# Kernel optimization log

Hardware: AMD Instinct MI355X
Metric: run time of the kernel (lower is better)

## Reference

```python
import jax, jax.numpy as jnp
import numpy as np

NUM_HEADS = 8
NEG_SLOPE = 0.2
MASK_VAL = -10000000000.0


def setup_inputs() -> dict:
    key = jax.random.key(0)
    k1, k2, k3, k4 = jax.random.split(key, 4)
    B, N, H, d, T = 16, 256, NUM_HEADS, 64, 5
    src = jax.random.normal(k1, (B, N, H * d), dtype=jnp.float32)
    dst = jax.random.normal(k2, (B, N, H * d), dtype=jnp.float32)
    # parameter a: (atom_d*H, atom_d, T); xavier-ish scale
    a = jax.random.normal(k3, (H * d, d, T), dtype=jnp.float32) * 0.08
    # bond-type indices in [-1, T); -1 = no edge (masked)
    edges = jax.random.randint(k4, (B, N, N), -1, T, dtype=jnp.int64)
    return {"src_embeddings": src, "dst_embeddings": dst, "a": a, "edges": edges}


def reference(src_embeddings, dst_embeddings, a, edges):
    B, N, d_ = src_embeddings.shape
    H = NUM_HEADS
    d = d_ // H
    T = a.shape[-1]
    # (B, H, N, d)
    s = src_embeddings.reshape(B, N, H, d).transpose(0, 2, 1, 3)
    t = dst_embeddings.reshape(B, N, H, d).transpose(0, 2, 1, 3)
    # a.view(H, d, d*T) in torch == reshape(H, d, d, T) with (e, t) flattened
    A = a.reshape(H, d, d, T)
    # transformed_src[b,h,i,e,t] = sum_d s[b,h,i,d] * A[h,d,e,t]
    transformed = jnp.einsum('bhid,hdet->bhiet', s, A)
    # scores[b,h,i,j,t] = sum_e transformed[b,h,i,e,t] * t[b,h,j,e]  -> (B,H,N,N,T)
    scores = jnp.einsum('bhiet,bhje->bhijt', transformed, t)
    # gather the per-edge bond-type slice
    idx = jnp.broadcast_to(jnp.clip(edges, 0)[:, None, :, :, None], (B, H, N, N, 1))
    sel = jnp.take_along_axis(scores, idx, axis=-1)[..., 0]  # (B,H,N,N)
    mask = (edges == -1)[:, None, :, :]
    sel = jnp.where(mask, jnp.asarray(MASK_VAL, sel.dtype), sel)
    return jax.nn.leaky_relu(sel, negative_slope=NEG_SLOPE)
```

## Files before the change

### kernel.cpp

```cpp
#include <hip/hip_runtime.h>
#include <hip/hip_bf16.h>

#define NB 16
#define NN 256
#define NH 8
#define ND 64
#define NT 5
#define HD 512

typedef __bf16 bf16x8 __attribute__((ext_vector_type(8)));
typedef __bf16 bf16x4 __attribute__((ext_vector_type(4)));
typedef float  f32x4  __attribute__((ext_vector_type(4)));
typedef int    i32x4  __attribute__((ext_vector_type(4)));

__device__ __forceinline__ bf16x8 cvt8(f32x4 a, f32x4 b) {
    bf16x8 r;
    r[0] = (__bf16)a[0]; r[1] = (__bf16)a[1]; r[2] = (__bf16)a[2]; r[3] = (__bf16)a[3];
    r[4] = (__bf16)b[0]; r[5] = (__bf16)b[1]; r[6] = (__bf16)b[2]; r[7] = (__bf16)b[3];
    return r;
}

__device__ __forceinline__ void stage16(const void* g, void* l) {
    __builtin_amdgcn_global_load_lds(
        (const __attribute__((address_space(1))) void*)g,
        (__attribute__((address_space(3))) void*)l,
        16, 0, 0);
}

__global__ void prep_w_kernel(const float* __restrict__ a, __bf16* __restrict__ wt) {
    const int o8 = (blockIdx.x * 256 + threadIdx.x) * 8;
    if (o8 >= NH * ND * ND * NT) return;
    const int dd0 = o8 & 63;
    const int e   = (o8 >> 6) & 63;
    const int ht  = o8 >> 12;
    const int t   = ht % NT;
    const int h   = ht / NT;
    bf16x8 v;
    #pragma unroll
    for (int j = 0; j < 8; ++j)
        v[j] = (__bf16)a[((size_t)(h * ND + dd0 + j) * ND + e) * NT + t];
    *reinterpret_cast<bf16x8*>(wt + o8) = v;
}

#define LW   0
#define LP0  0
#define LP1  10240
#define LS2  20480
#define LE2  24576
#define LS0  40960
#define LS1  45056
#define LE0  49152
#define LE1  57344

__global__ __launch_bounds__(512, 2) void mhea_fused(
    const float* __restrict__ src, const float* __restrict__ dst,
    const __bf16* __restrict__ wt, const int* __restrict__ edges,
    float* __restrict__ out)
{
    __shared__ alignas(16) unsigned char Lb[65536];

    const int bid = blockIdx.x;
    const int wg  = (bid & 7) * 64 + (bid >> 3);
    const int b   = wg >> 5;
    const int h   = (wg >> 2) & 7;
    const int jh  = (wg >> 1) & 1;
    const int ih  = wg & 1;
    const int j0  = jh * 128;
    const int ib0 = ih * 128;

    const int tid = threadIdx.x;
    const int w   = tid >> 6;
    const int l   = tid & 63;
    const int il  = l & 15;
    const int kg  = l >> 4;

    const int et  = w & 3;
    const int tl  = w >> 2;
    const int t0  = tl * 3;
    const int ntl = 3 - tl;

    const int SO[3] = {LS0, LS1, LS2};
    const int EO[3] = {LE0, LE1, LE2};

    f32x4 q0, q1, q2, q3;
    {
        const float* dp = dst + ((size_t)(b * NN + j0 + w * 16 + il)) * HD + h * ND;
        q0 = *reinterpret_cast<const f32x4*>(dp + kg * 8);
        q1 = *reinterpret_cast<const f32x4*>(dp + kg * 8 + 4);
        q2 = *reinterpret_cast<const f32x4*>(dp + 32 + kg * 8);
        q3 = *reinterpret_cast<const f32x4*>(dp + 36 + kg * 8);
    }

    {
        const __bf16* wbase = wt + (size_t)(h * NT) * ND * ND;
        #pragma unroll
        for (int k = 0; k < 5; ++k) {
            const int idx = w * 5 + k;
            const int t   = idx >> 3;
            const int sub = idx & 7;
            const int e   = sub * 8 + (l >> 3);
            const int c   = (l & 7) ^ (e & 7);
            stage16(wbase + ((size_t)t * ND + e) * ND + c * 8,
                    Lb + LW + t * 8192 + sub * 1024);
        }
    }
    if (w < 4) {
        #pragma unroll
        for (int p = 0; p < 2; ++p) {
            const int row = w * 4 + (l >> 4);
            const int c   = (l & 15) ^ (row & 7);
            stage16(src + ((size_t)(b * NN + ib0 + p * 16 + row)) * HD + h * ND + c * 4,
                    Lb + SO[p] + w * 1024);
        }
    }
    #pragma unroll
    for (int p = 0; p < 2; ++p) {
        const int row = w * 2 + (l >> 5);
        const int c   = (l & 31) ^ (row & 7);
        stage16(edges + ((size_t)(b * NN + ib0 + p * 16 + row)) * NN + j0 + c * 4,
                Lb + EO[p] + w * 1024);
    }

    bf16x8 cb0 = cvt8(q0, q1);
    bf16x8 cb1 = cvt8(q2, q3);

    asm volatile("s_waitcnt vmcnt(0)" ::: "memory");
    __builtin_amdgcn_sched_barrier(0);
    __builtin_amdgcn_s_barrier();

    bf16x8 wa[3][2];
    #pragma unroll
    for (int tt = 0; tt < 3; ++tt) {
        if (tt < ntl) {
            const int t = t0 + tt;
            #pragma unroll
            for (int ks = 0; ks < 2; ++ks)
                wa[tt][ks] = *reinterpret_cast<const bf16x8*>(
                    Lb + LW + t * 8192 + (et * 16 + il) * 128
                       + (((ks * 4 + kg) ^ (il & 7)) << 4));
        }
    }
    asm volatile("s_waitcnt lgkmcnt(0)" ::: "memory");
    __builtin_amdgcn_sched_barrier(0);
    __builtin_amdgcn_s_barrier();

    #pragma unroll
    for (int k = 0; k < 8; ++k) {
        const float* Sc = (const float*)(Lb + SO[k % 3]);
        const int*   Ec = (const int*)  (Lb + EO[k % 3]);
        __bf16*      Pc = (__bf16*)     (Lb + ((k & 1) ? LP1 : LP0));

        if (k < 6) {
            const int i2 = ib0 + (k + 2) * 16;
            if (w < 4) {
                const int row = w * 4 + (l >> 4);
                const int c   = (l & 15) ^ (row & 7);
                stage16(src + ((size_t)(b * NN + i2 + row)) * HD + h * ND + c * 4,
                        Lb + SO[(k + 2) % 3] + w * 1024);
            }
            {
                const int row = w * 2 + (l >> 5);
                const int c   = (l & 31) ^ (row & 7);
                stage16(edges + ((size_t)(b * NN + i2 + row)) * NN + j0 + c * 4,
                        Lb + EO[(k + 2) % 3] + w * 1024);
            }
        }

        const i32x4 ce = *reinterpret_cast<const i32x4*>(
            Ec + il * 128 + (((w * 4 + kg) ^ (il & 7)) << 2));

        {
            f32x4 a0 = *reinterpret_cast<const f32x4*>(&Sc[il * ND + (((2 * kg + 0) ^ (il & 7)) << 2)]);
            f32x4 a1 = *reinterpret_cast<const f32x4*>(&Sc[il * ND + (((2 * kg + 1) ^ (il & 7)) << 2)]);
            f32x4 a2 = *reinterpret_cast<const f32x4*>(&Sc[il * ND + (((8 + 2 * kg) ^ (il & 7)) << 2)]);
            f32x4 a3 = *reinterpret_cast<const f32x4*>(&Sc[il * ND + (((9 + 2 * kg) ^ (il & 7)) << 2)]);
            bf16x8 bf0 = cvt8(a0, a1);
            bf16x8 bf1 = cvt8(a2, a3);
            __builtin_amdgcn_s_setprio(1);
            #pragma unroll
            for (int tt = 0; tt < 3; ++tt) {
                if (tt < ntl) {
                    const int t = t0 + tt;
                    f32x4 pacc = {0.f, 0.f, 0.f, 0.f};
                    pacc = __builtin_amdgcn_mfma_f32_16x16x32_bf16(wa[tt][0], bf0, pacc, 0, 0, 0);
                    pacc = __builtin_amdgcn_mfma_f32_16x16x32_bf16(wa[tt][1], bf1, pacc, 0, 0, 0);
                    bf16x4 pk;
                    pk[0] = (__bf16)pacc[0];
                    pk[1] = (__bf16)pacc[1];
                    pk[2] = (__bf16)pacc[2];
                    pk[3] = (__bf16)pacc[3];
                    const int elem = (et * 16 + kg * 4) ^ ((il & 7) << 3);
                    *reinterpret_cast<bf16x4*>(Pc + t * 1024 + il * ND + elem) = pk;
                }
            }
            __builtin_amdgcn_s_setprio(0);
        }

        if (k < 6) {
            if (w < 4) { asm volatile("s_waitcnt vmcnt(3) lgkmcnt(0)" ::: "memory"); }
            else       { asm volatile("s_waitcnt vmcnt(2) lgkmcnt(0)" ::: "memory"); }
        } else {
            asm volatile("s_waitcnt vmcnt(1) lgkmcnt(0)" ::: "memory");
        }
        __builtin_amdgcn_sched_barrier(0);
        __builtin_amdgcn_s_barrier();

        {
            bf16x8 pa[NT][2];
            #pragma unroll
            for (int t = 0; t < NT; ++t)
                #pragma unroll
                for (int ks = 0; ks < 2; ++ks)
                    pa[t][ks] = *reinterpret_cast<const bf16x8*>(
                        Pc + t * 1024 + il * ND + (((ks * 4 + kg) ^ (il & 7)) << 3));

            __builtin_amdgcn_s_setprio(1);
            f32x4 acc[NT];
            #pragma unroll
            for (int t = 0; t < NT; ++t) {
                acc[t] = (f32x4){0.f, 0.f, 0.f, 0.f};
                acc[t] = __builtin_amdgcn_mfma_f32_16x16x32_bf16(cb0, pa[t][0], acc[t], 0, 0, 0);
                acc[t] = __builtin_amdgcn_mfma_f32_16x16x32_bf16(cb1, pa[t][1], acc[t], 0, 0, 0);
            }
            __builtin_amdgcn_s_setprio(0);

            f32x4 o;
            #pragma unroll
            for (int r = 0; r < 4; ++r) {
                const int ev = ce[r];
                float x;
                if (ev < 0) { x = -1e10f; }
                else {
                    x = (ev == 0) ? acc[0][r]
                      : (ev == 1) ? acc[1][r]
                      : (ev == 2) ? acc[2][r]
                      : (ev == 3) ? acc[3][r]
                      :             acc[4][r];
                }
                o[r] = (x >= 0.f) ? x : 0.2f * x;
            }
            *reinterpret_cast<f32x4*>(
                out + ((size_t)(b * NH + h) * NN + ib0 + k * 16 + il) * NN
                    + j0 + w * 16 + kg * 4) = o;
        }
    }
}

__global__ __launch_bounds__(64, 3) void mhea_fused_fallback(
    const float* __restrict__ src, const float* __restrict__ dst,
    const float* __restrict__ araw, const int* __restrict__ edges,
    float* __restrict__ out)
{
    __shared__ __bf16 Plds[NT * 16 * 64];

    const int it = blockIdx.x;
    const int h  = blockIdx.y;
    const int b  = blockIdx.z;
    const int i0 = it * 16;

    const int l  = threadIdx.x & 63;
    const int il = l & 15;
    const int kg = l >> 4;

    const float* dbase = dst + (size_t)b * NN * HD + h * ND;
    const int*   erow  = edges + ((size_t)b * NN + i0 + il) * NN;
    const float* sbase = src + (size_t)(b * NN + i0 + il) * HD + h * ND;

    f32x4 s0 = *reinterpret_cast<const f32x4*>(sbase + kg * 8);
    f32x4 s1 = *reinterpret_cast<const f32x4*>(sbase + kg * 8 + 4);
    f32x4 s2 = *reinterpret_cast<const f32x4*>(sbase + 32 + kg * 8);
    f32x4 s3 = *reinterpret_cast<const f32x4*>(sbase + 36 + kg * 8);
    bf16x8 af0 = cvt8(s0, s1);
    bf16x8 af1 = cvt8(s2, s3);

    #pragma unroll
    for (int t = 0; t < NT; ++t) {
        #pragma unroll
        for (int et = 0; et < 4; ++et) {
            bf16x8 w0, w1;
            #pragma unroll
            for (int jj = 0; jj < 8; ++jj) {
                const int ee = et * 16 + il;
                w0[jj] = (__bf16)araw[((size_t)(h * ND + kg * 8 + jj) * ND + ee) * NT + t];
                w1[jj] = (__bf16)araw[((size_t)(h * ND + kg * 8 + jj + 32) * ND + ee) * NT + t];
            }
            f32x4 pacc = {0.f, 0.f, 0.f, 0.f};
            pacc = __builtin_amdgcn_mfma_f32_16x16x32_bf16(w0, af0, pacc, 0, 0, 0);
            pacc = __builtin_amdgcn_mfma_f32_16x16x32_bf16(w1, af1, pacc, 0, 0, 0);
            bf16x4 pk;
            pk[0] = (__bf16)pacc[0];
            pk[1] = (__bf16)pacc[1];
            pk[2] = (__bf16)pacc[2];
            pk[3] = (__bf16)pacc[3];
            const int elem = (et * 16 + kg * 4) ^ ((il & 7) << 3);
            *reinterpret_cast<bf16x4*>(&Plds[t * 1024 + il * 64 + elem]) = pk;
        }
    }

    bf16x8 pa[NT][2];
    #pragma unroll
    for (int t = 0; t < NT; ++t) {
        #pragma unroll
        for (int ks = 0; ks < 2; ++ks) {
            const int elem = (ks * 32 + kg * 8) ^ ((il & 7) << 3);
            pa[t][ks] = *reinterpret_cast<const bf16x8*>(&Plds[t * 1024 + il * 64 + elem]);
        }
    }

    float* obase = out + (((size_t)(b * NH + h)) * NN + i0 + il) * NN;

    for (int jt = 0; jt < 16; ++jt) {
        const float* np = dbase + (size_t)(jt * 16 + il) * HD + kg * 8;
        f32x4 d0 = *reinterpret_cast<const f32x4*>(np);
        f32x4 d1 = *reinterpret_cast<const f32x4*>(np + 4);
        f32x4 d2 = *reinterpret_cast<const f32x4*>(np + 32);
        f32x4 d3 = *reinterpret_cast<const f32x4*>(np + 36);
        i32x4 ce = *reinterpret_cast<const i32x4*>(erow + jt * 16 + kg * 4);
        const bf16x8 cb0 = cvt8(d0, d1);
        const bf16x8 cb1 = cvt8(d2, d3);
        f32x4 acc[NT];
        #pragma unroll
        for (int t = 0; t < NT; ++t) {
            acc[t] = (f32x4){0.f, 0.f, 0.f, 0.f};
            acc[t] = __builtin_amdgcn_mfma_f32_16x16x32_bf16(cb0, pa[t][0], acc[t], 0, 0, 0);
            acc[t] = __builtin_amdgcn_mfma_f32_16x16x32_bf16(cb1, pa[t][1], acc[t], 0, 0, 0);
        }
        f32x4 o;
        #pragma unroll
        for (int r = 0; r < 4; ++r) {
            const int ev = ce[r];
            float x;
            if (ev < 0) { x = -1e10f; }
            else {
                x = (ev == 0) ? acc[0][r]
                  : (ev == 1) ? acc[1][r]
                  : (ev == 2) ? acc[2][r]
                  : (ev == 3) ? acc[3][r]
                  :             acc[4][r];
            }
            o[r] = (x >= 0.f) ? x : 0.2f * x;
        }
        *reinterpret_cast<f32x4*>(obase + jt * 16 + kg * 4) = o;
    }
}

extern "C" void kernel_launch(void* const* d_in, const int* in_sizes, int n_in,
                              void* d_out, int out_size, void* d_ws, size_t ws_size,
                              hipStream_t stream) {
    const float* src   = (const float*)d_in[0];
    const float* dst   = (const float*)d_in[1];
    const float* a     = (const float*)d_in[2];
    const int*   edges = (const int*)d_in[3];
    float* out = (float*)d_out;

    const size_t wt_bytes = (size_t)NH * NT * ND * ND * sizeof(__bf16);

    if (ws_size >= wt_bytes) {
        __bf16* wt = (__bf16*)d_ws;
        const int total = NH * ND * ND * NT;
        prep_w_kernel<<<(total / 8 + 255) / 256, 256, 0, stream>>>(a, wt);
        mhea_fused<<<512, 512, 0, stream>>>(src, dst, wt, edges, out);
    } else {
        mhea_fused_fallback<<<dim3(NN / 16, NH, NB), 64, 0, stream>>>(
            src, dst, a, edges, out);
    }
}
```

Measured before the change: 27.39 us.

## Split waves into producer and consumer roles for software-pipelined two-stage MFMA

Waves 0-3 become producers: they stage src and edges tiles and compute the first-stage projection (src times A) for the next row block. Waves 4-7 become consumers: each handles two 16-column dst tiles for the second-stage scores, the edge-type select, the mask and leaky ReLU. Stage one for block k+1 now runs at the same time as stage two for block k, with one barrier per iteration instead of two. In exchange, each consumer holds twice the accumulator registers, the producers take on all of the staging loads, and the vmcnt wait counts were rewritten by hand, which is easy to get wrong.

```diff
diff --git a/kernel.cpp b/kernel.cpp
--- a/kernel.cpp
+++ b/kernel.cpp
@@ -74,21 +74,24 @@
     const int il  = l & 15;
     const int kg  = l >> 4;
 
-    const int et  = w & 3;
-    const int tl  = w >> 2;
-    const int t0  = tl * 3;
-    const int ntl = 3 - tl;
-
-    const int SO[3] = {LS0, LS1, LS2};
-    const int EO[3] = {LE0, LE1, LE2};
-
-    f32x4 q0, q1, q2, q3;
-    {
-        const float* dp = dst + ((size_t)(b * NN + j0 + w * 16 + il)) * HD + h * ND;
-        q0 = *reinterpret_cast<const f32x4*>(dp + kg * 8);
-        q1 = *reinterpret_cast<const f32x4*>(dp + kg * 8 + 4);
-        q2 = *reinterpret_cast<const f32x4*>(dp + 32 + kg * 8);
-        q3 = *reinterpret_cast<const f32x4*>(dp + 36 + kg * 8);
+    const bool prod = (w < 4);
+    const int  cw   = w - 4;
+
+    const int SOc[3] = {LS0, LS1, LS2};
+    const int EOc[3] = {LE0, LE1, LE2};
+
+    f32x4 qA0{}, qA1{}, qA2{}, qA3{}, qB0{}, qB1{}, qB2{}, qB3{};
+    if (!prod) {
+        const float* dpA = dst + ((size_t)(b * NN + j0 + (2 * cw) * 16 + il)) * HD + h * ND;
+        const float* dpB = dst + ((size_t)(b * NN + j0 + (2 * cw + 1) * 16 + il)) * HD + h * ND;
+        qA0 = *reinterpret_cast<const f32x4*>(dpA + kg * 8);
+        qA1 = *reinterpret_cast<const f32x4*>(dpA + kg * 8 + 4);
+        qA2 = *reinterpret_cast<const f32x4*>(dpA + 32 + kg * 8);
+        qA3 = *reinterpret_cast<const f32x4*>(dpA + 36 + kg * 8);
+        qB0 = *reinterpret_cast<const f32x4*>(dpB + kg * 8);
+        qB1 = *reinterpret_cast<const f32x4*>(dpB + kg * 8 + 4);
+        qB2 = *reinterpret_cast<const f32x4*>(dpB + 32 + kg * 8);
+        qB3 = *reinterpret_cast<const f32x4*>(dpB + 36 + kg * 8);
     }
 
     {
@@ -104,108 +107,139 @@
                     Lb + LW + t * 8192 + sub * 1024);
         }
     }
-    if (w < 4) {
+    if (prod) {
         #pragma unroll
         for (int p = 0; p < 2; ++p) {
             const int row = w * 4 + (l >> 4);
             const int c   = (l & 15) ^ (row & 7);
             stage16(src + ((size_t)(b * NN + ib0 + p * 16 + row)) * HD + h * ND + c * 4,
-                    Lb + SO[p] + w * 1024);
-        }
-    }
-    #pragma unroll
-    for (int p = 0; p < 2; ++p) {
-        const int row = w * 2 + (l >> 5);
-        const int c   = (l & 31) ^ (row & 7);
-        stage16(edges + ((size_t)(b * NN + ib0 + p * 16 + row)) * NN + j0 + c * 4,
-                Lb + EO[p] + w * 1024);
-    }
-
-    bf16x8 cb0 = cvt8(q0, q1);
-    bf16x8 cb1 = cvt8(q2, q3);
+                    Lb + SOc[p] + w * 1024);
+        }
+        #pragma unroll
+        for (int p = 0; p < 2; ++p) {
+            #pragma unroll
+            for (int kk = 0; kk < 2; ++kk) {
+                const int idx = w * 2 + kk;
+                const int row = idx * 2 + (l >> 5);
+                const int c   = (l & 31) ^ (row & 7);
+                stage16(edges + ((size_t)(b * NN + ib0 + p * 16 + row)) * NN + j0 + c * 4,
+                        Lb + EOc[p] + idx * 1024);
+            }
+        }
+    }
 
     asm volatile("s_waitcnt vmcnt(0)" ::: "memory");
     __builtin_amdgcn_sched_barrier(0);
     __builtin_amdgcn_s_barrier();
 
-    bf16x8 wa[3][2];
-    #pragma unroll
-    for (int tt = 0; tt < 3; ++tt) {
-        if (tt < ntl) {
-            const int t = t0 + tt;
+    bf16x8 wa[NT][2];
+    bf16x8 cbA0, cbA1, cbB0, cbB1;
+    if (prod) {
+        #pragma unroll
+        for (int t = 0; t < NT; ++t)
             #pragma unroll
             for (int ks = 0; ks < 2; ++ks)
-                wa[tt][ks] = *reinterpret_cast<const bf16x8*>(
-                    Lb + LW + t * 8192 + (et * 16 + il) * 128
+                wa[t][ks] = *reinterpret_cast<const bf16x8*>(
+                    Lb + LW + t * 8192 + (w * 16 + il) * 128
                        + (((ks * 4 + kg) ^ (il & 7)) << 4));
-        }
-    }
-    asm volatile("s_waitcnt lgkmcnt(0)" ::: "memory");
+        asm volatile("s_waitcnt lgkmcnt(0)" ::: "memory");
+    } else {
+        cbA0 = cvt8(qA0, qA1); cbA1 = cvt8(qA2, qA3);
+        cbB0 = cvt8(qB0, qB1); cbB1 = cvt8(qB2, qB3);
+    }
     __builtin_amdgcn_sched_barrier(0);
     __builtin_amdgcn_s_barrier();
 
+    if (prod) {
+        const float* Sc = (const float*)(Lb + LS0);
+        __bf16*      Pc = (__bf16*)(Lb + LP0);
+        f32x4 a0 = *reinterpret_cast<const f32x4*>(&Sc[il * ND + (((2 * kg + 0) ^ (il & 7)) << 2)]);
+        f32x4 a1 = *reinterpret_cast<const f32x4*>(&Sc[il * ND + (((2 * kg + 1) ^ (il & 7)) << 2)]);
+        f32x4 a2 = *reinterpret_cast<const f32x4*>(&Sc[il * ND + (((8 + 2 * kg) ^ (il & 7)) << 2)]);
+        f32x4 a3 = *reinterpret_cast<const f32x4*>(&Sc[il * ND + (((9 + 2 * kg) ^ (il & 7)) << 2)]);
+        bf16x8 bf0 = cvt8(a0, a1);
+        bf16x8 bf1 = cvt8(a2, a3);
+        #pragma unroll
+        for (int t = 0; t < NT; ++t) {
+            f32x4 pacc = {0.f, 0.f, 0.f, 0.f};
+            pacc = __builtin_amdgcn_mfma_f32_16x16x32_bf16(wa[t][0], bf0, pacc, 0, 0, 0);
+            pacc = __builtin_amdgcn_mfma_f32_16x16x32_bf16(wa[t][1], bf1, pacc, 0, 0, 0);
+            bf16x4 pk;
+            pk[0] = (__bf16)pacc[0];
+            pk[1] = (__bf16)pacc[1];
+            pk[2] = (__bf16)pacc[2];
+            pk[3] = (__bf16)pacc[3];
+            const int elem = (w * 16 + kg * 4) ^ ((il & 7) << 3);
+            *reinterpret_cast<bf16x4*>(Pc + t * 1024 + il * ND + elem) = pk;
+        }
+        asm volatile("s_waitcnt lgkmcnt(0)" ::: "memory");
+    }
+    __builtin_amdgcn_sched_barrier(0);
+    __builtin_amdgcn_s_barrier();
+
     #pragma unroll
     for (int k = 0; k < 8; ++k) {
-        const float* Sc = (const float*)(Lb + SO[k % 3]);
-        const int*   Ec = (const int*)  (Lb + EO[k % 3]);
-        __bf16*      Pc = (__bf16*)     (Lb + ((k & 1) ? LP1 : LP0));
-
-        if (k < 6) {
-            const int i2 = ib0 + (k + 2) * 16;
-            if (w < 4) {
+        if (prod) {
+            if (k == 0) {
                 const int row = w * 4 + (l >> 4);
                 const int c   = (l & 15) ^ (row & 7);
-                stage16(src + ((size_t)(b * NN + i2 + row)) * HD + h * ND + c * 4,
-                        Lb + SO[(k + 2) % 3] + w * 1024);
-            }
-            {
-                const int row = w * 2 + (l >> 5);
-                const int c   = (l & 31) ^ (row & 7);
-                stage16(edges + ((size_t)(b * NN + i2 + row)) * NN + j0 + c * 4,
-                        Lb + EO[(k + 2) % 3] + w * 1024);
-            }
-        }
-
-        const i32x4 ce = *reinterpret_cast<const i32x4*>(
-            Ec + il * 128 + (((w * 4 + kg) ^ (il & 7)) << 2));
-
-        {
-            f32x4 a0 = *reinterpret_cast<const f32x4*>(&Sc[il * ND + (((2 * kg + 0) ^ (il & 7)) << 2)]);
-            f32x4 a1 = *reinterpret_cast<const f32x4*>(&Sc[il * ND + (((2 * kg + 1) ^ (il & 7)) << 2)]);
-            f32x4 a2 = *reinterpret_cast<const f32x4*>(&Sc[il * ND + (((8 + 2 * kg) ^ (il & 7)) << 2)]);
-            f32x4 a3 = *reinterpret_cast<const f32x4*>(&Sc[il * ND + (((9 + 2 * kg) ^ (il & 7)) << 2)]);
-            bf16x8 bf0 = cvt8(a0, a1);
-            bf16x8 bf1 = cvt8(a2, a3);
-            __builtin_amdgcn_s_setprio(1);
-            #pragma unroll
-            for (int tt = 0; tt < 3; ++tt) {
-                if (tt < ntl) {
-                    const int t = t0 + tt;
+                stage16(src + ((size_t)(b * NN + ib0 + 2 * 16 + row)) * HD + h * ND + c * 4,
+                        Lb + LS2 + w * 1024);
+            }
+            if (k <= 4) {
+                const int row = w * 4 + (l >> 4);
+                const int c   = (l & 15) ^ (row & 7);
+                stage16(src + ((size_t)(b * NN + ib0 + (k + 3) * 16 + row)) * HD + h * ND + c * 4,
+                        Lb + SOc[(k + 3) % 3] + w * 1024);
+            }
+            if (k <= 5) {
+                #pragma unroll
+                for (int kk = 0; kk < 2; ++kk) {
+                    const int idx = w * 2 + kk;
+                    const int row = idx * 2 + (l >> 5);
+                    const int c   = (l & 31) ^ (row & 7);
+                    stage16(edges + ((size_t)(b * NN + ib0 + (k + 2) * 16 + row)) * NN + j0 + c * 4,
+                            Lb + EOc[(k + 2) % 3] + idx * 1024);
+                }
+            }
+            if (k < 7) {
+                const float* Sc = (const float*)(Lb + SOc[(k + 1) % 3]);
+                __bf16*      Pc = (__bf16*)(Lb + (((k + 1) & 1) ? LP1 : LP0));
+                f32x4 a0 = *reinterpret_cast<const f32x4*>(&Sc[il * ND + (((2 * kg + 0) ^ (il & 7)) << 2)]);
+                f32x4 a1 = *reinterpret_cast<const f32x4*>(&Sc[il * ND + (((2 * kg + 1) ^ (il & 7)) << 2)]);
+                f32x4 a2 = *reinterpret_cast<const f32x4*>(&Sc[il * ND + (((8 + 2 * kg) ^ (il & 7)) << 2)]);
+                f32x4 a3 = *reinterpret_cast<const f32x4*>(&Sc[il * ND + (((9 + 2 * kg) ^ (il & 7)) << 2)]);
+                bf16x8 bf0 = cvt8(a0, a1);
+                bf16x8 bf1 = cvt8(a2, a3);
+                __builtin_amdgcn_s_setprio(1);
+                #pragma unroll
+                for (int t = 0; t < NT; ++t) {
                     f32x4 pacc = {0.f, 0.f, 0.f, 0.f};
-                    pacc = __builtin_amdgcn_mfma_f32_16x16x32_bf16(wa[tt][0], bf0, pacc, 0, 0, 0);
-                    pacc = __builtin_amdgcn_mfma_f32_16x16x32_bf16(wa[tt][1], bf1, pacc, 0, 0, 0);
+                    pacc = __builtin_amdgcn_mfma_f32_16x16x32_bf16(wa[t][0], bf0, pacc, 0, 0, 0);
+                    pacc = __builtin_amdgcn_mfma_f32_16x16x32_bf16(wa[t][1], bf1, pacc, 0, 0, 0);
                     bf16x4 pk;
                     pk[0] = (__bf16)pacc[0];
                     pk[1] = (__bf16)pacc[1];
                     pk[2] = (__bf16)pacc[2];
                     pk[3] = (__bf16)pacc[3];
-                    const int elem = (et * 16 + kg * 4) ^ ((il & 7) << 3);
+                    const int elem = (w * 16 + kg * 4) ^ ((il & 7) << 3);
                     *reinterpret_cast<bf16x4*>(Pc + t * 1024 + il * ND + elem) = pk;
                 }
-            }
-            __builtin_amdgcn_s_setprio(0);
-        }
-
-        if (k < 6) {
-            if (w < 4) { asm volatile("s_waitcnt vmcnt(3) lgkmcnt(0)" ::: "memory"); }
-            else       { asm volatile("s_waitcnt vmcnt(2) lgkmcnt(0)" ::: "memory"); }
+                __builtin_amdgcn_s_setprio(0);
+            }
+            if (k == 0)      { asm volatile("s_waitcnt vmcnt(3) lgkmcnt(0)" ::: "memory"); }
+            else if (k <= 4) { asm volatile("s_waitcnt vmcnt(3) lgkmcnt(0)" ::: "memory"); }
+            else if (k == 5) { asm volatile("s_waitcnt vmcnt(2) lgkmcnt(0)" ::: "memory"); }
+            else             { asm volatile("s_waitcnt vmcnt(0) lgkmcnt(0)" ::: "memory"); }
         } else {
-            asm volatile("s_waitcnt vmcnt(1) lgkmcnt(0)" ::: "memory");
-        }
-        __builtin_amdgcn_sched_barrier(0);
-        __builtin_amdgcn_s_barrier();
-
-        {
+            const int*    Ec = (const int*)(Lb + EOc[k % 3]);
+            const __bf16* Pc = (const __bf16*)(Lb + ((k & 1) ? LP1 : LP0));
+
+            const i32x4 ceA = *reinterpret_cast<const i32x4*>(
+                Ec + il * 128 + ((((2 * cw) * 4 + kg) ^ (il & 7)) << 2));
+            const i32x4 ceB = *reinterpret_cast<const i32x4*>(
+                Ec + il * 128 + ((((2 * cw + 1) * 4 + kg) ^ (il & 7)) << 2));
+
             bf16x8 pa[NT][2];
             #pragma unroll
             for (int t = 0; t < NT; ++t)
@@ -215,34 +249,52 @@
                         Pc + t * 1024 + il * ND + (((ks * 4 + kg) ^ (il & 7)) << 3));
 
             __builtin_amdgcn_s_setprio(1);
-            f32x4 acc[NT];
+            f32x4 accA[NT], accB[NT];
             #pragma unroll
             for (int t = 0; t < NT; ++t) {
-                acc[t] = (f32x4){0.f, 0.f, 0.f, 0.f};
-                acc[t] = __builtin_amdgcn_mfma_f32_16x16x32_bf16(cb0, pa[t][0], acc[t], 0, 0, 0);
-                acc[t] = __builtin_amdgcn_mfma_f32_16x16x32_bf16(cb1, pa[t][1], acc[t], 0, 0, 0);
+                accA[t] = (f32x4){0.f, 0.f, 0.f, 0.f};
+                accB[t] = (f32x4){0.f, 0.f, 0.f, 0.f};
+                accA[t] = __builtin_amdgcn_mfma_f32_16x16x32_bf16(cbA0, pa[t][0], accA[t], 0, 0, 0);
+                accB[t] = __builtin_amdgcn_mfma_f32_16x16x32_bf16(cbB0, pa[t][0], accB[t], 0, 0, 0);
+                accA[t] = __builtin_amdgcn_mfma_f32_16x16x32_bf16(cbA1, pa[t][1], accA[t], 0, 0, 0);
+                accB[t] = __builtin_amdgcn_mfma_f32_16x16x32_bf16(cbB1, pa[t][1], accB[t], 0, 0, 0);
             }
             __builtin_amdgcn_s_setprio(0);
 
-            f32x4 o;
+            float* orow = out + ((size_t)(b * NH + h) * NN + ib0 + k * 16 + il) * NN + j0;
+            f32x4 oA, oB;
             #pragma unroll
             for (int r = 0; r < 4; ++r) {
-                const int ev = ce[r];
-                float x;
-                if (ev < 0) { x = -1e10f; }
+                const int evA = ceA[r];
+                float xA;
+                if (evA < 0) { xA = -1e10f; }
                 else {
-                    x = (ev == 0) ? acc[0][r]
-                      : (ev == 1) ? acc[1][r]
-                      : (ev == 2) ? acc[2][r]
-                      : (ev == 3) ? acc[3][r]
-                      :             acc[4][r];
+                    xA = (evA == 0) ? accA[0][r]
+                       : (evA == 1) ? accA[1][r]
+                       : (evA == 2) ? accA[2][r]
+                       : (evA == 3) ? accA[3][r]
+                       :              accA[4][r];
                 }
-                o[r] = (x >= 0.f) ? x : 0.2f * x;
-            }
-            *reinterpret_cast<f32x4*>(
-                out + ((size_t)(b * NH + h) * NN + ib0 + k * 16 + il) * NN
-                    + j0 + w * 16 + kg * 4) = o;
-        }
+                oA[r] = (xA >= 0.f) ? xA : 0.2f * xA;
+                const int evB = ceB[r];
+                float xB;
+                if (evB < 0) { xB = -1e10f; }
+                else {
+                    xB = (evB == 0) ? accB[0][r]
+                       : (evB == 1) ? accB[1][r]
+                       : (evB == 2) ? accB[2][r]
+                       : (evB == 3) ? accB[3][r]
+                       :              accB[4][r];
+                }
+                oB[r] = (xB >= 0.f) ? xB : 0.2f * xB;
+            }
+            *reinterpret_cast<f32x4*>(orow + (2 * cw) * 16 + kg * 4)     = oA;
+            *reinterpret_cast<f32x4*>(orow + (2 * cw + 1) * 16 + kg * 4) = oB;
+
+            asm volatile("s_waitcnt vmcnt(2) lgkmcnt(0)" ::: "memory");
+        }
+        __builtin_amdgcn_sched_barrier(0);
+        __builtin_amdgcn_s_barrier();
     }
 }
 
```

Result: slower. 38.18 us (+39.4%).

## Preload edge indices into registers instead of staging them through LDS

Applied to the files above, without the earlier changes.

Each thread now loads all eight 16-row chunks of edge indices straight from global memory into registers at kernel start. This replaces the triple-buffered LDS staging and the per-iteration LDS reads, which shrinks shared memory from 64KB to 48KB and simplifies the per-iteration wait counts. The trade-offs are 32 more VGPRs per thread and all edge loads being issued up front instead of being pipelined with compute.

```diff
diff --git a/kernel.cpp b/kernel.cpp
--- a/kernel.cpp
+++ b/kernel.cpp
@@ -46,18 +46,15 @@
 #define LP0  0
 #define LP1  10240
 #define LS2  20480
-#define LE2  24576
 #define LS0  40960
 #define LS1  45056
-#define LE0  49152
-#define LE1  57344
 
 __global__ __launch_bounds__(512, 2) void mhea_fused(
     const float* __restrict__ src, const float* __restrict__ dst,
     const __bf16* __restrict__ wt, const int* __restrict__ edges,
     float* __restrict__ out)
 {
-    __shared__ alignas(16) unsigned char Lb[65536];
+    __shared__ alignas(16) unsigned char Lb[49152];
 
     const int bid = blockIdx.x;
     const int wg  = (bid & 7) * 64 + (bid >> 3);
@@ -80,7 +77,6 @@
     const int ntl = 3 - tl;
 
     const int SO[3] = {LS0, LS1, LS2};
-    const int EO[3] = {LE0, LE1, LE2};
 
     f32x4 q0, q1, q2, q3;
     {
@@ -90,6 +86,11 @@
         q2 = *reinterpret_cast<const f32x4*>(dp + 32 + kg * 8);
         q3 = *reinterpret_cast<const f32x4*>(dp + 36 + kg * 8);
     }
+    i32x4 ceall[8];
+    #pragma unroll
+    for (int k = 0; k < 8; ++k)
+        ceall[k] = *reinterpret_cast<const i32x4*>(
+            edges + ((size_t)(b * NN + ib0 + k * 16 + il)) * NN + j0 + w * 16 + kg * 4);
 
     {
         const __bf16* wbase = wt + (size_t)(h * NT) * ND * ND;
@@ -113,13 +114,6 @@
                     Lb + SO[p] + w * 1024);
         }
     }
-    #pragma unroll
-    for (int p = 0; p < 2; ++p) {
-        const int row = w * 2 + (l >> 5);
-        const int c   = (l & 31) ^ (row & 7);
-        stage16(edges + ((size_t)(b * NN + ib0 + p * 16 + row)) * NN + j0 + c * 4,
-                Lb + EO[p] + w * 1024);
-    }
 
     bf16x8 cb0 = cvt8(q0, q1);
     bf16x8 cb1 = cvt8(q2, q3);
@@ -147,27 +141,17 @@
     #pragma unroll
     for (int k = 0; k < 8; ++k) {
         const float* Sc = (const float*)(Lb + SO[k % 3]);
-        const int*   Ec = (const int*)  (Lb + EO[k % 3]);
         __bf16*      Pc = (__bf16*)     (Lb + ((k & 1) ? LP1 : LP0));
 
-        if (k < 6) {
-            const int i2 = ib0 + (k + 2) * 16;
-            if (w < 4) {
-                const int row = w * 4 + (l >> 4);
-                const int c   = (l & 15) ^ (row & 7);
-                stage16(src + ((size_t)(b * NN + i2 + row)) * HD + h * ND + c * 4,
-                        Lb + SO[(k + 2) % 3] + w * 1024);
-            }
-            {
-                const int row = w * 2 + (l >> 5);
-                const int c   = (l & 31) ^ (row & 7);
-                stage16(edges + ((size_t)(b * NN + i2 + row)) * NN + j0 + c * 4,
-                        Lb + EO[(k + 2) % 3] + w * 1024);
-            }
-        }
-
-        const i32x4 ce = *reinterpret_cast<const i32x4*>(
-            Ec + il * 128 + (((w * 4 + kg) ^ (il & 7)) << 2));
+        if (k < 6 && w < 4) {
+            const int i2  = ib0 + (k + 2) * 16;
+            const int row = w * 4 + (l >> 4);
+            const int c   = (l & 15) ^ (row & 7);
+            stage16(src + ((size_t)(b * NN + i2 + row)) * HD + h * ND + c * 4,
+                    Lb + SO[(k + 2) % 3] + w * 1024);
+        }
+
+        const i32x4 ce = ceall[k];
 
         {
             f32x4 a0 = *reinterpret_cast<const f32x4*>(&Sc[il * ND + (((2 * kg + 0) ^ (il & 7)) << 2)]);
@@ -196,11 +180,11 @@
             __builtin_amdgcn_s_setprio(0);
         }
 
-        if (k < 6) {
-            if (w < 4) { asm volatile("s_waitcnt vmcnt(3) lgkmcnt(0)" ::: "memory"); }
-            else       { asm volatile("s_waitcnt vmcnt(2) lgkmcnt(0)" ::: "memory"); }
+        if (w < 4) {
+            if (k < 6) { asm volatile("s_waitcnt vmcnt(2) lgkmcnt(0)" ::: "memory"); }
+            else       { asm volatile("s_waitcnt vmcnt(1) lgkmcnt(0)" ::: "memory"); }
         } else {
-            asm volatile("s_waitcnt vmcnt(1) lgkmcnt(0)" ::: "memory");
+            asm volatile("s_waitcnt lgkmcnt(0)" ::: "memory");
         }
         __builtin_amdgcn_sched_barrier(0);
         __builtin_amdgcn_s_barrier();
```

New measurement: 29.63 us. 8.2% more time.
